# Optimization experiments

Measured on AMD Instinct MI355X. Metric: run time of the kernel, lower is better.

The kernel has to match this reference:

```python
import math
import jax, jax.numpy as jnp
import numpy as np

H, D, HID, BLOCK = 32, 64, 2048, 256   # heads, head_dim, hidden(=h*d), chunk size
N = 8192                                # prefill sequence length
NUM_LAYERS, LAYER_IDX = 80, 0
EPS = 1e-5


def _build_slopes(n):
    def p2(m):
        start = 2 ** (-2 ** (-(math.log2(m) - 3)))
        return [start * start ** i for i in range(m)]
    if math.log2(n).is_integer():
        s = p2(n)
    else:
        cp = 2 ** math.floor(math.log2(n))
        s = p2(cp) + _build_slopes(2 * cp).tolist()[0::2][: n - cp]
    return np.array(s, dtype=np.float32)

SLOPE = jnp.asarray(_build_slopes(H) * (1.0 - LAYER_IDX / (NUM_LAYERS - 1) + 1e-5))  # [H]


def setup_inputs() -> dict:
    key = jax.random.key(0)
    ks = jax.random.split(key, 5)
    return {
        "hidden_states": jax.random.normal(ks[0], (N, HID), jnp.float32),
        "kv_cache": jnp.zeros((H, D, D), jnp.float32),
        "W_qkv": jax.random.normal(ks[1], (3 * HID, HID), jnp.float32) * 0.02,
        "W_gate": jax.random.normal(ks[2], (HID, HID), jnp.float32) * 0.02,
        "W_out": jax.random.normal(ks[3], (HID, HID), jnp.float32) * 0.02,
        "norm_weight": jnp.ones((HID,), jnp.float32),
    }


def lightning_attention(q, k, v, slope, kv0):
    # q,k,v: [h,n,d]; kv0: [h,d,d]; chunked linear attention with per-head decay
    h, n, d = q.shape
    nb = n // BLOCK
    arr = jnp.arange(BLOCK, dtype=jnp.float32) + 1.0          # 1..BLOCK
    s = slope[:, None, None]                                   # [h,1,1]
    q_decay = jnp.exp(-s * arr[None, :, None])                 # [h,B,1]
    k_decay = jnp.exp(-s * (BLOCK - arr)[None, :, None])       # [h,B,1]
    idx = arr[:, None] - arr[None, :]                          # [B,B]
    diag_decay = jnp.where(idx[None] >= 0, jnp.exp(-s * idx[None]), 0.0)  # [h,B,B]
    block_decay = jnp.exp(-slope * BLOCK)[:, None, None]       # [h,1,1]

    def to_blocks(x):
        return x.reshape(h, nb, BLOCK, d).transpose(1, 0, 2, 3)  # [nb,h,B,d]

    qb, kb, vb = to_blocks(q), to_blocks(k), to_blocks(v)

    def step(kv, blk):
        qi, ki, vi = blk                                        # [h,B,d]
        inter = jnp.einsum('hmd,hde->hme', qi * q_decay, kv)    # carry-state term
        qk = jnp.einsum('hmd,hnd->hmn', qi, ki) * diag_decay    # intra-block causal decayed scores
        intra = jnp.einsum('hmn,hne->hme', qk, vi)
        kv_new = block_decay * kv + jnp.einsum('hmd,hme->hde', ki * k_decay, vi)
        return kv_new, inter + intra

    kv_final, out = jax.lax.scan(step, kv0, (qb, kb, vb))
    out = out.transpose(1, 0, 2, 3).reshape(h, n, d)
    return out, kv_final


def reference(hidden_states, kv_cache, W_qkv, W_gate, W_out, norm_weight):
    # qkv projection + SiLU in fp32 (as in vLLM MiniMaxText01)
    qkv = jax.nn.silu((hidden_states @ W_qkv.T).astype(jnp.float32))  # [n, 3*HID]
    qkv = qkv.reshape(N, H, 3 * D)
    q, k, v = jnp.split(qkv, 3, axis=-1)                              # each [n,h,d]
    q, k, v = (t.transpose(1, 0, 2) for t in (q, k, v))               # [h,n,d]
    attn, _kv = lightning_attention(q, k, v, SLOPE, kv_cache)
    hidden = attn.transpose(1, 0, 2).reshape(N, H * D)                # 'h n d -> n (h d)'
    # RMSNorm (tp_world=1)
    var = jnp.mean(hidden * hidden, axis=-1, keepdims=True)
    hidden = hidden * jax.lax.rsqrt(var + EPS) * norm_weight
    gate = jax.nn.sigmoid(hidden_states @ W_gate.T)
    return (gate * hidden) @ W_out.T
```

## Files before the change

### kernel.cpp

```cpp
#include <hip/hip_runtime.h>

#define NTOK   8192
#define HIDDEN 2048
#define NHEAD  32
#define HDIM   64
#define BLK    256
#define NBLK   32
#define QKVW   6144

typedef unsigned short ushort_t;
typedef __attribute__((ext_vector_type(8))) short bf16x8;
typedef __attribute__((ext_vector_type(4))) float floatx4;
typedef __attribute__((ext_vector_type(4))) unsigned short ushortx4;

#define MFMA16(a, b, c) __builtin_amdgcn_mfma_f32_16x16x32_bf16(a, b, c, 0, 0, 0)

__device__ __forceinline__ float head_slope(int h) {
    return exp2f(-0.25f * (float)(h + 1)) * 1.00001f;
}

__device__ __forceinline__ ushort_t f2bf(float x) {
    unsigned int u = __float_as_uint(x);
    unsigned int r = (u + 0x7FFFu + ((u >> 16) & 1u)) >> 16;
    return (ushort_t)r;
}
__device__ __forceinline__ float bf2f(ushort_t x) {
    return __uint_as_float(((unsigned int)x) << 16);
}
__device__ __forceinline__ void store1(float* p, float v) { *p = v; }
__device__ __forceinline__ void store1(ushort_t* p, float v) { *p = f2bf(v); }

#define GLOAD_LDS16(g, l)                                              \
    __builtin_amdgcn_global_load_lds(                                  \
        (const __attribute__((address_space(1))) void*)(g),            \
        (__attribute__((address_space(3))) void*)(l), 16, 0, 0)

__global__ __launch_bounds__(256) void cvt_bf16(
    const float* __restrict__ in, ushort_t* __restrict__ out, int n8) {
    int i = blockIdx.x * 256 + threadIdx.x;
    if (i >= n8) return;
    long base = (long)i * 8;
    float4 a = *(const float4*)(in + base);
    float4 b = *(const float4*)(in + base + 4);
    ushort4 u0 = {f2bf(a.x), f2bf(a.y), f2bf(a.z), f2bf(a.w)};
    ushort4 u1 = {f2bf(b.x), f2bf(b.y), f2bf(b.z), f2bf(b.w)};
    *(ushort4*)(out + base) = u0;
    *(ushort4*)(out + base + 4) = u1;
}

template <int EPI, typename OutT>
__global__ __launch_bounds__(512, 2) void gemm256_bt(
    const ushort_t* __restrict__ A, const ushort_t* __restrict__ B,
    OutT* __restrict__ C, const float* __restrict__ Mul,
    int M, int Ncol, int K) {
    __shared__ __align__(128) ushort_t As[3][256 * 32];
    __shared__ __align__(128) ushort_t Bs[3][256 * 32];

    const int t = threadIdx.x;
    const int wave = t >> 6, lane = t & 63;
    const int wm = wave >> 2, wn = wave & 3;
    const int fm = lane & 15, quad = lane >> 4;
    const int pcol = (quad ^ ((fm >> 1) & 3)) << 3;

    const int nbn = Ncol >> 8;
    const int flat = blockIdx.y * gridDim.x + blockIdx.x;
    const int nwg = gridDim.x * gridDim.y;
    const int nid = (flat & 7) * (nwg >> 3) + (flat >> 3);
    const int bm = nid / nbn, bn = nid % nbn;

    const int sr = t >> 2;
    const int sc = (((t & 3) ^ ((t >> 3) & 3))) << 3;
    const ushort_t* Ag0 = A + (long)(bm * 256 + sr) * K + sc;
    const ushort_t* Ag1 = Ag0 + (long)128 * K;
    const ushort_t* Bg0 = B + (long)(bn * 256 + sr) * K + sc;
    const ushort_t* Bg1 = Bg0 + (long)128 * K;
    const int ldst = wave * 512;

#define STAGE256(kt_, buf_)                                            \
    do {                                                               \
        const long ko_ = (long)(kt_) * 32;                             \
        GLOAD_LDS16(Ag0 + ko_, &As[buf_][ldst]);                       \
        GLOAD_LDS16(Ag1 + ko_, &As[buf_][4096 + ldst]);                \
        GLOAD_LDS16(Bg0 + ko_, &Bs[buf_][ldst]);                       \
        GLOAD_LDS16(Bg1 + ko_, &Bs[buf_][4096 + ldst]);                \
    } while (0)

    floatx4 acc[8][4];
#pragma unroll
    for (int i = 0; i < 8; i++)
#pragma unroll
        for (int j = 0; j < 4; j++) acc[i][j] = (floatx4){0.f, 0.f, 0.f, 0.f};

    const int NKT = K >> 5;
    STAGE256(0, 0);
    STAGE256(1, 1);
    asm volatile("s_waitcnt vmcnt(4)" ::: "memory");
    __builtin_amdgcn_s_barrier();

    int cur = 0;
    for (int kt = 0; kt < NKT; ++kt) {
        const ushort_t* Ab = As[cur];
        const ushort_t* Bb = Bs[cur];
        int sb = cur + 2; if (sb >= 3) sb -= 3;
        const bool do_stage = (kt + 2 < NKT);

        bf16x8 af[4], bfr[4];
#pragma unroll
        for (int mt = 0; mt < 4; ++mt)
            af[mt] = *(const bf16x8*)&Ab[(wm * 128 + mt * 16 + fm) * 32 + pcol];
#pragma unroll
        for (int nt = 0; nt < 4; ++nt)
            bfr[nt] = *(const bf16x8*)&Bb[(wn * 64 + nt * 16 + fm) * 32 + pcol];
        if (do_stage) {
            const long ko = (long)(kt + 2) * 32;
            GLOAD_LDS16(Ag0 + ko, &As[sb][ldst]);
            GLOAD_LDS16(Ag1 + ko, &As[sb][4096 + ldst]);
        }
        asm volatile("s_waitcnt lgkmcnt(0)" ::: "memory");
        __builtin_amdgcn_sched_barrier(0);
        __builtin_amdgcn_s_setprio(1);
#pragma unroll
        for (int mt = 0; mt < 4; ++mt)
#pragma unroll
            for (int nt = 0; nt < 4; ++nt)
                acc[mt][nt] = MFMA16(af[mt], bfr[nt], acc[mt][nt]);
        __builtin_amdgcn_s_setprio(0);
        __builtin_amdgcn_s_barrier();

#pragma unroll
        for (int mt = 0; mt < 4; ++mt)
            af[mt] = *(const bf16x8*)&Ab[(wm * 128 + 64 + mt * 16 + fm) * 32 + pcol];
        if (do_stage) {
            const long ko = (long)(kt + 2) * 32;
            GLOAD_LDS16(Bg0 + ko, &Bs[sb][ldst]);
            GLOAD_LDS16(Bg1 + ko, &Bs[sb][4096 + ldst]);
        }
        asm volatile("s_waitcnt lgkmcnt(0)" ::: "memory");
        __builtin_amdgcn_sched_barrier(0);
        __builtin_amdgcn_s_setprio(1);
#pragma unroll
        for (int mt = 0; mt < 4; ++mt)
#pragma unroll
            for (int nt = 0; nt < 4; ++nt)
                acc[4 + mt][nt] = MFMA16(af[mt], bfr[nt], acc[4 + mt][nt]);
        __builtin_amdgcn_s_setprio(0);

        if (kt + 2 < NKT) {
            asm volatile("s_waitcnt vmcnt(4)" ::: "memory");
            __builtin_amdgcn_s_barrier();
        } else if (kt + 1 < NKT) {
            asm volatile("s_waitcnt vmcnt(0)" ::: "memory");
            __builtin_amdgcn_s_barrier();
        }
        cur = sb - 1; if (cur < 0) cur = 2;
    }
#undef STAGE256

#pragma unroll
    for (int mh = 0; mh < 2; ++mh)
#pragma unroll
        for (int mt = 0; mt < 4; ++mt)
#pragma unroll
            for (int nt = 0; nt < 4; ++nt) {
                long col = (long)bn * 256 + wn * 64 + nt * 16 + fm;
#pragma unroll
                for (int r = 0; r < 4; ++r) {
                    long row = (long)bm * 256 + wm * 128 + mh * 64 + mt * 16 +
                               quad * 4 + r;
                    long idx = row * Ncol + col;
                    float x = acc[mh * 4 + mt][nt][r];
                    float o;
                    if (EPI == 0)      o = x / (1.f + expf(-x));
                    else if (EPI == 1) o = x;
                    else               o = Mul[idx] / (1.f + expf(-x));
                    store1(C + idx, o);
                }
            }
}

__global__ __launch_bounds__(256) void attn_contrib_mfma(
    const ushort_t* __restrict__ qkv, float* __restrict__ contrib) {
    const int b = blockIdx.x, h = blockIdx.y;
    const float s = head_slope(h);
    __shared__ ushort_t kdT[64][72];
    __shared__ ushort_t vT[64][72];
    const int t = threadIdx.x, wave = t >> 6, lane = t & 63;
    const int fm = lane & 15, quad = lane >> 4;
    const ushort_t* base = qkv + (long)(b * BLK) * QKVW + h * (3 * HDIM);

    floatx4 acc[4];
#pragma unroll
    for (int e = 0; e < 4; e++) acc[e] = (floatx4){0.f, 0.f, 0.f, 0.f};

    const int sn = t & 63;
    const int sc0 = t >> 6;

    for (int tt = 0; tt < 4; tt++) {
        __syncthreads();
        int tok = tt * 64 + sn;
        float kd = expf(-s * (float)(BLK - 1 - tok));
#pragma unroll
        for (int cc = 0; cc < 2; cc++) {
            int c = sc0 + cc * 4;
            bf16x8 k8 = *(const bf16x8*)(base + (long)tok * QKVW + HDIM + c * 8);
            bf16x8 v8 = *(const bf16x8*)(base + (long)tok * QKVW + 2 * HDIM + c * 8);
#pragma unroll
            for (int j = 0; j < 8; j++) {
                kdT[c * 8 + j][sn] = f2bf(bf2f((ushort_t)k8[j]) * kd);
                vT[c * 8 + j][sn]  = (ushort_t)v8[j];
            }
        }
        __syncthreads();
#pragma unroll
        for (int kh = 0; kh < 2; kh++) {
            bf16x8 a = *(const bf16x8*)&kdT[wave * 16 + fm][kh * 32 + quad * 8];
#pragma unroll
            for (int e = 0; e < 4; e++) {
                bf16x8 bb = *(const bf16x8*)&vT[e * 16 + fm][kh * 32 + quad * 8];
                acc[e] = MFMA16(a, bb, acc[e]);
            }
        }
    }
    float* outp = contrib + ((long)(h * NBLK + b)) * 4096;
#pragma unroll
    for (int e = 0; e < 4; e++)
#pragma unroll
        for (int r = 0; r < 4; r++) {
            int d = wave * 16 + quad * 4 + r;
            outp[d * 64 + e * 16 + fm] = acc[e][r];
        }
}

__global__ __launch_bounds__(256) void attn_scan(
    const float* __restrict__ kv0, const float* __restrict__ contrib,
    float* __restrict__ states) {
    const int h = blockIdx.x, t = threadIdx.x;
    const float s  = head_slope(h);
    const float bd = expf(-s * (float)BLK);
    float st[16], c[16];
    const float* kvp = kv0 + (long)h * 4096;
#pragma unroll
    for (int i = 0; i < 16; i++) st[i] = kvp[t + 256 * i];
    for (int b = 0; b < NBLK; b++) {
        const float* cp = contrib + ((long)(h * NBLK + b)) * 4096;
        float* sp = states + ((long)(h * NBLK + b)) * 4096;
#pragma unroll
        for (int i = 0; i < 16; i++) c[i] = cp[t + 256 * i];
#pragma unroll
        for (int i = 0; i < 16; i++) sp[t + 256 * i] = st[i];
#pragma unroll
        for (int i = 0; i < 16; i++) st[i] = bd * st[i] + c[i];
    }
}

__global__ __launch_bounds__(256) void attn_core_mfma(
    const ushort_t* __restrict__ qkv, const float* __restrict__ states,
    float* __restrict__ hidden) {
    const int b = blockIdx.x, h = blockIdx.y;
    const float s = head_slope(h);
    __shared__ ushort_t Sw[4][64][72];
    __shared__ ushort_t kS[64 * 64];
    __shared__ ushort_t vT[64][72];
    __shared__ float dtab[257];
    __shared__ float etab[64];
    const int t = threadIdx.x, wave = t >> 6, lane = t & 63;
    const int fm = lane & 15, quad = lane >> 4;
    const ushort_t* base = qkv + (long)(b * BLK) * QKVW + h * (3 * HDIM);

    dtab[t] = expf(-s * (float)t);
    if (t == 0) dtab[256] = expf(-s * 256.f);
    if (t < 64) etab[t] = expf(s * (float)t);

    {
        const float* sp = states + ((long)(h * NBLK + b)) * 4096;
#pragma unroll
        for (int i = 0; i < 4; i++) {
            int idx = t + 256 * i;
            int d = idx >> 4, e4 = (idx & 15) * 4;
            float4 st4 = *(const float4*)(sp + d * 64 + e4);
            Sw[0][e4 + 0][d] = f2bf(st4.x);
            Sw[0][e4 + 1][d] = f2bf(st4.y);
            Sw[0][e4 + 2][d] = f2bf(st4.z);
            Sw[0][e4 + 3][d] = f2bf(st4.w);
        }
    }

    bf16x8 aq[4][2];
#pragma unroll
    for (int mt = 0; mt < 4; mt++)
#pragma unroll
        for (int kh = 0; kh < 2; kh++)
            aq[mt][kh] = *(const bf16x8*)(base +
                (long)(wave * 64 + mt * 16 + fm) * QKVW + kh * 32 + quad * 8);

    __syncthreads();

    floatx4 acc[4][4];
#pragma unroll
    for (int i = 0; i < 4; i++)
#pragma unroll
        for (int j = 0; j < 4; j++) acc[i][j] = (floatx4){0.f, 0.f, 0.f, 0.f};
#pragma unroll
    for (int kh = 0; kh < 2; kh++)
#pragma unroll
        for (int et = 0; et < 4; et++) {
            bf16x8 bst = *(const bf16x8*)&Sw[0][et * 16 + fm][kh * 32 + quad * 8];
#pragma unroll
            for (int mt = 0; mt < 4; mt++)
                acc[mt][et] = MFMA16(aq[mt][kh], bst, acc[mt][et]);
        }
#pragma unroll
    for (int mt = 0; mt < 4; mt++)
#pragma unroll
        for (int r = 0; r < 4; r++) {
            float qd = dtab[wave * 64 + mt * 16 + quad * 4 + r + 1];
#pragma unroll
            for (int et = 0; et < 4; et++) acc[mt][et][r] *= qd;
        }

    const int sn = t & 63, sc0 = t >> 6;
    for (int nt = 0; nt < 4; nt++) {
        __syncthreads();
#pragma unroll
        for (int i = 0; i < 2; i++) {
            int row = i * 32 + wave * 8 + (lane >> 3);
            const ushort_t* g = base + (long)(nt * 64 + row) * QKVW + HDIM +
                                (((lane & 7) ^ (lane >> 3)) * 8);
            GLOAD_LDS16(g, &kS[(i * 32 + wave * 8) * 64]);
        }
#pragma unroll
        for (int cc = 0; cc < 2; cc++) {
            int c = sc0 + cc * 4;
            bf16x8 v8 = *(const bf16x8*)(base + (long)(nt * 64 + sn) * QKVW +
                                         2 * HDIM + c * 8);
#pragma unroll
            for (int j = 0; j < 8; j++) vT[c * 8 + j][sn] = (ushort_t)v8[j];
        }
        __syncthreads();

        if (nt <= wave) {
            floatx4 sacc[4][4];
#pragma unroll
            for (int i = 0; i < 4; i++)
#pragma unroll
                for (int j = 0; j < 4; j++) sacc[i][j] = (floatx4){0.f, 0.f, 0.f, 0.f};
#pragma unroll
            for (int kh = 0; kh < 2; kh++) {
                bf16x8 ak[4];
#pragma unroll
                for (int snt = 0; snt < 4; snt++) {
                    int n = snt * 16 + fm;
                    int pos = (kh * 4 + quad) ^ (n & 7);
                    ak[snt] = *(const bf16x8*)&kS[n * 64 + pos * 8];
                }
#pragma unroll
                for (int snt = 0; snt < 4; snt++)
#pragma unroll
                    for (int smt = 0; smt < 4; smt++)
                        sacc[snt][smt] = MFMA16(ak[snt], aq[smt][kh], sacc[snt][smt]);
            }
#pragma unroll
            for (int snt = 0; snt < 4; snt++)
#pragma unroll
                for (int smt = 0; smt < 4; smt++) {
                    int mloc = smt * 16 + fm;
                    float rf = dtab[wave * 64 + mloc - nt * 64];
                    ushortx4 o;
#pragma unroll
                    for (int r = 0; r < 4; r++) {
                        int nloc = snt * 16 + quad * 4 + r;
                        float v = sacc[snt][smt][r] * rf * etab[nloc];
                        if (nt == wave && mloc < nloc) v = 0.f;
                        o[r] = f2bf(v);
                    }
                    *(ushortx4*)&Sw[wave][mloc][snt * 16 + quad * 4] = o;
                }
#pragma unroll
            for (int kh = 0; kh < 2; kh++) {
                bf16x8 as[4];
#pragma unroll
                for (int mt = 0; mt < 4; mt++)
                    as[mt] = *(const bf16x8*)&Sw[wave][mt * 16 + fm][kh * 32 + quad * 8];
#pragma unroll
                for (int et = 0; et < 4; et++) {
                    bf16x8 bv = *(const bf16x8*)&vT[et * 16 + fm][kh * 32 + quad * 8];
#pragma unroll
                    for (int mt = 0; mt < 4; mt++)
                        acc[mt][et] = MFMA16(as[mt], bv, acc[mt][et]);
                }
            }
        }
    }

#pragma unroll
    for (int mt = 0; mt < 4; mt++)
#pragma unroll
        for (int r = 0; r < 4; r++) {
            long tok = (long)b * BLK + wave * 64 + mt * 16 + quad * 4 + r;
            float* hp = hidden + tok * HIDDEN + h * HDIM;
#pragma unroll
            for (int et = 0; et < 4; et++)
                hp[et * 16 + fm] = acc[mt][et][r];
        }
}

__global__ __launch_bounds__(256) void rmsnorm_rows(
    float* __restrict__ hidden, const float* __restrict__ w) {
    const int row = blockIdx.x, t = threadIdx.x;
    float* hp = hidden + (long)row * HIDDEN;
    float4 a = *(const float4*)(hp + (t << 2));
    float4 b = *(const float4*)(hp + 1024 + (t << 2));
    float ss = a.x * a.x + a.y * a.y + a.z * a.z + a.w * a.w +
               b.x * b.x + b.y * b.y + b.z * b.z + b.w * b.w;
#pragma unroll
    for (int off = 32; off > 0; off >>= 1) ss += __shfl_down(ss, off);
    __shared__ float red[4];
    if ((t & 63) == 0) red[t >> 6] = ss;
    __syncthreads();
    float tot = red[0] + red[1] + red[2] + red[3];
    float scale = rsqrtf(tot * (1.f / HIDDEN) + 1e-5f);
    float4 wa = *(const float4*)(w + (t << 2));
    float4 wb = *(const float4*)(w + 1024 + (t << 2));
    a.x *= scale * wa.x; a.y *= scale * wa.y; a.z *= scale * wa.z; a.w *= scale * wa.w;
    b.x *= scale * wb.x; b.y *= scale * wb.y; b.z *= scale * wb.z; b.w *= scale * wb.w;
    *(float4*)(hp + (t << 2)) = a;
    *(float4*)(hp + 1024 + (t << 2)) = b;
}

extern "C" void kernel_launch(void* const* d_in, const int* in_sizes, int n_in,
                              void* d_out, int out_size, void* d_ws, size_t ws_size,
                              hipStream_t stream) {
    (void)in_sizes; (void)n_in; (void)out_size; (void)ws_size;
    const float* hs   = (const float*)d_in[0];
    const float* kv0  = (const float*)d_in[1];
    const float* Wqkv = (const float*)d_in[2];
    const float* Wg   = (const float*)d_in[3];
    const float* Wo   = (const float*)d_in[4];
    const float* nw   = (const float*)d_in[5];
    float* out = (float*)d_out;

    ushort_t* hs_h   = (ushort_t*)d_ws;
    ushort_t* wqkv_h = hs_h + (size_t)NTOK * HIDDEN;
    ushort_t* wg_h   = wqkv_h + (size_t)QKVW * HIDDEN;
    ushort_t* wo_h   = wg_h + (size_t)HIDDEN * HIDDEN;
    ushort_t* qkv_h  = wo_h + (size_t)HIDDEN * HIDDEN;
    float*    cs     = (float*)(qkv_h + (size_t)NTOK * QKVW);
    ushort_t* gated  = qkv_h;

    cvt_bf16<<<(NTOK * HIDDEN / 8 + 255) / 256, 256, 0, stream>>>(
        hs, hs_h, NTOK * HIDDEN / 8);
    cvt_bf16<<<(QKVW * HIDDEN / 8 + 255) / 256, 256, 0, stream>>>(
        Wqkv, wqkv_h, QKVW * HIDDEN / 8);
    cvt_bf16<<<(HIDDEN * HIDDEN / 8 + 255) / 256, 256, 0, stream>>>(
        Wg, wg_h, HIDDEN * HIDDEN / 8);
    cvt_bf16<<<(HIDDEN * HIDDEN / 8 + 255) / 256, 256, 0, stream>>>(
        Wo, wo_h, HIDDEN * HIDDEN / 8);

    gemm256_bt<0, ushort_t><<<dim3(QKVW / 256, NTOK / 256), 512, 0, stream>>>(
        hs_h, wqkv_h, qkv_h, nullptr, NTOK, QKVW, HIDDEN);
    attn_contrib_mfma<<<dim3(NBLK, NHEAD), 256, 0, stream>>>(qkv_h, cs);
    attn_scan<<<NHEAD, 256, 0, stream>>>(kv0, cs, cs);
    attn_core_mfma<<<dim3(NBLK, NHEAD), 256, 0, stream>>>(qkv_h, cs, out);
    rmsnorm_rows<<<NTOK, 256, 0, stream>>>(out, nw);
    gemm256_bt<2, ushort_t><<<dim3(HIDDEN / 256, NTOK / 256), 512, 0, stream>>>(
        hs_h, wg_h, gated, out, NTOK, HIDDEN, HIDDEN);
    gemm256_bt<1, float><<<dim3(HIDDEN / 256, NTOK / 256), 512, 0, stream>>>(
        gated, wo_h, out, nullptr, NTOK, HIDDEN, HIDDEN);
}
```

Before: 694.7 us.

## Deepen GEMM LDS pipeline to four stages and reorder tile rasterization

Moves the bf16 GEMM from a 3-buffer to a 4-buffer LDS ring, prefetching three k-tiles ahead with matching vmcnt waits and extra barriers, so global-load latency has more time to hide. It also changes the workgroup-to-tile mapping to walk M first within each column of B tiles, and fixes the LDS swizzle to use the row index. LDS use grows to 128KB per workgroup, which may fall short of the two workgroups per CU that the launch bounds ask for, and the added barriers cost extra synchronization per k-step.

```diff
diff --git a/kernel.cpp b/kernel.cpp
--- a/kernel.cpp
+++ b/kernel.cpp
@@ -53,8 +53,8 @@
     const ushort_t* __restrict__ A, const ushort_t* __restrict__ B,
     OutT* __restrict__ C, const float* __restrict__ Mul,
     int M, int Ncol, int K) {
-    __shared__ __align__(128) ushort_t As[3][256 * 32];
-    __shared__ __align__(128) ushort_t Bs[3][256 * 32];
+    __shared__ __align__(128) ushort_t As[4][256 * 32];
+    __shared__ __align__(128) ushort_t Bs[4][256 * 32];
 
     const int t = threadIdx.x;
     const int wave = t >> 6, lane = t & 63;
@@ -62,25 +62,30 @@
     const int fm = lane & 15, quad = lane >> 4;
     const int pcol = (quad ^ ((fm >> 1) & 3)) << 3;
 
-    const int nbn = Ncol >> 8;
     const int flat = blockIdx.y * gridDim.x + blockIdx.x;
     const int nwg = gridDim.x * gridDim.y;
     const int nid = (flat & 7) * (nwg >> 3) + (flat >> 3);
-    const int bm = nid / nbn, bn = nid % nbn;
+    const int nbm = M >> 8;
+    const int bn = nid / nbm;
+    const int bm = nid - bn * nbm;
 
     const int sr = t >> 2;
-    const int sc = (((t & 3) ^ ((t >> 3) & 3))) << 3;
+    const int sc = ((t & 3) ^ ((sr >> 1) & 3)) << 3;
     const ushort_t* Ag0 = A + (long)(bm * 256 + sr) * K + sc;
     const ushort_t* Ag1 = Ag0 + (long)128 * K;
     const ushort_t* Bg0 = B + (long)(bn * 256 + sr) * K + sc;
     const ushort_t* Bg1 = Bg0 + (long)128 * K;
     const int ldst = wave * 512;
 
-#define STAGE256(kt_, buf_)                                            \
+#define STAGE_A(kt_, buf_)                                             \
     do {                                                               \
         const long ko_ = (long)(kt_) * 32;                             \
         GLOAD_LDS16(Ag0 + ko_, &As[buf_][ldst]);                       \
         GLOAD_LDS16(Ag1 + ko_, &As[buf_][4096 + ldst]);                \
+    } while (0)
+#define STAGE_B(kt_, buf_)                                             \
+    do {                                                               \
+        const long ko_ = (long)(kt_) * 32;                             \
         GLOAD_LDS16(Bg0 + ko_, &Bs[buf_][ldst]);                       \
         GLOAD_LDS16(Bg1 + ko_, &Bs[buf_][4096 + ldst]);                \
     } while (0)
@@ -92,17 +97,17 @@
         for (int j = 0; j < 4; j++) acc[i][j] = (floatx4){0.f, 0.f, 0.f, 0.f};
 
     const int NKT = K >> 5;
-    STAGE256(0, 0);
-    STAGE256(1, 1);
-    asm volatile("s_waitcnt vmcnt(4)" ::: "memory");
+    STAGE_A(0, 0); STAGE_B(0, 0);
+    STAGE_A(1, 1); STAGE_B(1, 1);
+    STAGE_A(2, 2); STAGE_B(2, 2);
+    asm volatile("s_waitcnt vmcnt(8)" ::: "memory");
     __builtin_amdgcn_s_barrier();
 
-    int cur = 0;
     for (int kt = 0; kt < NKT; ++kt) {
-        const ushort_t* Ab = As[cur];
-        const ushort_t* Bb = Bs[cur];
-        int sb = cur + 2; if (sb >= 3) sb -= 3;
-        const bool do_stage = (kt + 2 < NKT);
+        const ushort_t* Ab = As[kt & 3];
+        const ushort_t* Bb = Bs[kt & 3];
+        const int sb = (kt + 3) & 3;
+        const bool do_stage = (kt + 3 < NKT);
 
         bf16x8 af[4], bfr[4];
 #pragma unroll
@@ -111,11 +116,8 @@
 #pragma unroll
         for (int nt = 0; nt < 4; ++nt)
             bfr[nt] = *(const bf16x8*)&Bb[(wn * 64 + nt * 16 + fm) * 32 + pcol];
-        if (do_stage) {
-            const long ko = (long)(kt + 2) * 32;
-            GLOAD_LDS16(Ag0 + ko, &As[sb][ldst]);
-            GLOAD_LDS16(Ag1 + ko, &As[sb][4096 + ldst]);
-        }
+        if (do_stage) STAGE_A(kt + 3, sb);
+        __builtin_amdgcn_s_barrier();
         asm volatile("s_waitcnt lgkmcnt(0)" ::: "memory");
         __builtin_amdgcn_sched_barrier(0);
         __builtin_amdgcn_s_setprio(1);
@@ -130,11 +132,8 @@
 #pragma unroll
         for (int mt = 0; mt < 4; ++mt)
             af[mt] = *(const bf16x8*)&Ab[(wm * 128 + 64 + mt * 16 + fm) * 32 + pcol];
-        if (do_stage) {
-            const long ko = (long)(kt + 2) * 32;
-            GLOAD_LDS16(Bg0 + ko, &Bs[sb][ldst]);
-            GLOAD_LDS16(Bg1 + ko, &Bs[sb][4096 + ldst]);
-        }
+        if (do_stage) STAGE_B(kt + 3, sb);
+        __builtin_amdgcn_s_barrier();
         asm volatile("s_waitcnt lgkmcnt(0)" ::: "memory");
         __builtin_amdgcn_sched_barrier(0);
         __builtin_amdgcn_s_setprio(1);
@@ -145,16 +144,17 @@
                 acc[4 + mt][nt] = MFMA16(af[mt], bfr[nt], acc[4 + mt][nt]);
         __builtin_amdgcn_s_setprio(0);
 
-        if (kt + 2 < NKT) {
+        if (kt + 3 < NKT) {
+            asm volatile("s_waitcnt vmcnt(8)" ::: "memory");
+        } else if (kt + 2 < NKT) {
             asm volatile("s_waitcnt vmcnt(4)" ::: "memory");
-            __builtin_amdgcn_s_barrier();
         } else if (kt + 1 < NKT) {
             asm volatile("s_waitcnt vmcnt(0)" ::: "memory");
-            __builtin_amdgcn_s_barrier();
-        }
-        cur = sb - 1; if (cur < 0) cur = 2;
+        }
+        __builtin_amdgcn_s_barrier();
     }
-#undef STAGE256
+#undef STAGE_A
+#undef STAGE_B
 
 #pragma unroll
     for (int mh = 0; mh < 2; ++mh)
```

Result: slower. 720.0 us (+3.6%).

## Restructure bf16 GEMM to K=64 tiles, double buffering and four-phase MFMA schedule

Applied to the files above, without the earlier changes.

The 256x256 bf16 GEMM mainloop now uses K-tiles of 64 instead of 32, with two LDS buffers instead of three and an XOR swizzle over 8 chunks. Each iteration is split into four MFMA quadrants, and the global-to-LDS loads for tile kt+2 are interleaved between quadrants so memory traffic overlaps compute and there are fewer loop iterations and barriers per K. The LDS footprint stays at 128KB. The cost is more barriers inside each iteration and a more fragile schedule, since the buffer being read is partly refilled while other quadrants still use it.

```diff
diff --git a/kernel.cpp b/kernel.cpp
--- a/kernel.cpp
+++ b/kernel.cpp
@@ -53,37 +53,38 @@
     const ushort_t* __restrict__ A, const ushort_t* __restrict__ B,
     OutT* __restrict__ C, const float* __restrict__ Mul,
     int M, int Ncol, int K) {
-    __shared__ __align__(128) ushort_t As[3][256 * 32];
-    __shared__ __align__(128) ushort_t Bs[3][256 * 32];
+    __shared__ __align__(128) ushort_t As[2][256 * 64];
+    __shared__ __align__(128) ushort_t Bs[2][256 * 64];
 
     const int t = threadIdx.x;
     const int wave = t >> 6, lane = t & 63;
     const int wm = wave >> 2, wn = wave & 3;
     const int fm = lane & 15, quad = lane >> 4;
-    const int pcol = (quad ^ ((fm >> 1) & 3)) << 3;
 
     const int nbn = Ncol >> 8;
     const int flat = blockIdx.y * gridDim.x + blockIdx.x;
     const int nwg = gridDim.x * gridDim.y;
     const int nid = (flat & 7) * (nwg >> 3) + (flat >> 3);
-    const int bm = nid / nbn, bn = nid % nbn;
-
-    const int sr = t >> 2;
-    const int sc = (((t & 3) ^ ((t >> 3) & 3))) << 3;
-    const ushort_t* Ag0 = A + (long)(bm * 256 + sr) * K + sc;
-    const ushort_t* Ag1 = Ag0 + (long)128 * K;
-    const ushort_t* Bg0 = B + (long)(bn * 256 + sr) * K + sc;
-    const ushort_t* Bg1 = Bg0 + (long)128 * K;
-    const int ldst = wave * 512;
-
-#define STAGE256(kt_, buf_)                                            \
-    do {                                                               \
-        const long ko_ = (long)(kt_) * 32;                             \
-        GLOAD_LDS16(Ag0 + ko_, &As[buf_][ldst]);                       \
-        GLOAD_LDS16(Ag1 + ko_, &As[buf_][4096 + ldst]);                \
-        GLOAD_LDS16(Bg0 + ko_, &Bs[buf_][ldst]);                       \
-        GLOAD_LDS16(Bg1 + ko_, &Bs[buf_][4096 + ldst]);                \
-    } while (0)
+    const int bm = nid / nbn;
+    const int bn = nid - bm * nbn;
+
+    const int srow = t >> 3;
+    const int schunk = ((t & 7) ^ (srow & 7)) << 3;
+    const ushort_t* Ags = A + ((long)bm * 256 + srow) * K + schunk;
+    const ushort_t* Bgs = B + ((long)bn * 256 + srow) * K + schunk;
+    const int sdst = wave * 512;
+
+#define STAGE_AQ(kt_, buf_, q_)                                          \
+    GLOAD_LDS16(Ags + (long)(q_) * 64 * K + (long)(kt_) * 64,            \
+                &As[buf_][(q_) * 4096 + sdst])
+#define STAGE_BQ(kt_, buf_, q_)                                          \
+    GLOAD_LDS16(Bgs + (long)(q_) * 64 * K + (long)(kt_) * 64,            \
+                &Bs[buf_][(q_) * 4096 + sdst])
+
+    const int aoff = (wm * 128 + fm) * 64;
+    const int boff = (wn * 64 + fm) * 64;
+    const int cx0 = ((quad ^ (fm & 7)) << 3);
+    const int cx1 = (((4 + quad) ^ (fm & 7)) << 3);
 
     floatx4 acc[8][4];
 #pragma unroll
@@ -91,91 +92,133 @@
 #pragma unroll
         for (int j = 0; j < 4; j++) acc[i][j] = (floatx4){0.f, 0.f, 0.f, 0.f};
 
-    const int NKT = K >> 5;
-    STAGE256(0, 0);
-    STAGE256(1, 1);
-    asm volatile("s_waitcnt vmcnt(4)" ::: "memory");
+    const int NKT = K >> 6;
+#pragma unroll
+    for (int q = 0; q < 4; q++) STAGE_AQ(0, 0, q);
+#pragma unroll
+    for (int q = 0; q < 4; q++) STAGE_BQ(0, 0, q);
+#pragma unroll
+    for (int q = 0; q < 4; q++) STAGE_AQ(1, 1, q);
+#pragma unroll
+    for (int q = 0; q < 4; q++) STAGE_BQ(1, 1, q);
+    asm volatile("s_waitcnt vmcnt(8)" ::: "memory");
     __builtin_amdgcn_s_barrier();
 
-    int cur = 0;
     for (int kt = 0; kt < NKT; ++kt) {
-        const ushort_t* Ab = As[cur];
-        const ushort_t* Bb = Bs[cur];
-        int sb = cur + 2; if (sb >= 3) sb -= 3;
-        const bool do_stage = (kt + 2 < NKT);
-
-        bf16x8 af[4], bfr[4];
-#pragma unroll
-        for (int mt = 0; mt < 4; ++mt)
-            af[mt] = *(const bf16x8*)&Ab[(wm * 128 + mt * 16 + fm) * 32 + pcol];
-#pragma unroll
-        for (int nt = 0; nt < 4; ++nt)
-            bfr[nt] = *(const bf16x8*)&Bb[(wn * 64 + nt * 16 + fm) * 32 + pcol];
-        if (do_stage) {
-            const long ko = (long)(kt + 2) * 32;
-            GLOAD_LDS16(Ag0 + ko, &As[sb][ldst]);
-            GLOAD_LDS16(Ag1 + ko, &As[sb][4096 + ldst]);
-        }
+        const int cur = kt & 1;
+        const ushort_t* Ab = &As[cur][0];
+        const ushort_t* Bb = &Bs[cur][0];
+        const bool st = (kt + 2 < NKT);
+
+        bf16x8 a0[4][2], a1[4][2], bl[2][2], bh[2][2];
+
+#pragma unroll
+        for (int mt = 0; mt < 4; ++mt) {
+            a0[mt][0] = *(const bf16x8*)&Ab[aoff + mt * 1024 + cx0];
+            a0[mt][1] = *(const bf16x8*)&Ab[aoff + mt * 1024 + cx1];
+        }
+#pragma unroll
+        for (int nt = 0; nt < 2; ++nt) {
+            bl[nt][0] = *(const bf16x8*)&Bb[boff + nt * 1024 + cx0];
+            bl[nt][1] = *(const bf16x8*)&Bb[boff + nt * 1024 + cx1];
+        }
+        __builtin_amdgcn_s_barrier();
         asm volatile("s_waitcnt lgkmcnt(0)" ::: "memory");
         __builtin_amdgcn_sched_barrier(0);
         __builtin_amdgcn_s_setprio(1);
 #pragma unroll
         for (int mt = 0; mt < 4; ++mt)
 #pragma unroll
-            for (int nt = 0; nt < 4; ++nt)
-                acc[mt][nt] = MFMA16(af[mt], bfr[nt], acc[mt][nt]);
+            for (int nt = 0; nt < 2; ++nt) {
+                acc[mt][nt] = MFMA16(a0[mt][0], bl[nt][0], acc[mt][nt]);
+                acc[mt][nt] = MFMA16(a0[mt][1], bl[nt][1], acc[mt][nt]);
+            }
         __builtin_amdgcn_s_setprio(0);
         __builtin_amdgcn_s_barrier();
 
 #pragma unroll
-        for (int mt = 0; mt < 4; ++mt)
-            af[mt] = *(const bf16x8*)&Ab[(wm * 128 + 64 + mt * 16 + fm) * 32 + pcol];
-        if (do_stage) {
-            const long ko = (long)(kt + 2) * 32;
-            GLOAD_LDS16(Bg0 + ko, &Bs[sb][ldst]);
-            GLOAD_LDS16(Bg1 + ko, &Bs[sb][4096 + ldst]);
-        }
+        for (int nt = 0; nt < 2; ++nt) {
+            bh[nt][0] = *(const bf16x8*)&Bb[boff + 2048 + nt * 1024 + cx0];
+            bh[nt][1] = *(const bf16x8*)&Bb[boff + 2048 + nt * 1024 + cx1];
+        }
+        if (st) { STAGE_AQ(kt + 2, cur, 0); STAGE_AQ(kt + 2, cur, 2); }
+        __builtin_amdgcn_s_barrier();
         asm volatile("s_waitcnt lgkmcnt(0)" ::: "memory");
         __builtin_amdgcn_sched_barrier(0);
         __builtin_amdgcn_s_setprio(1);
 #pragma unroll
         for (int mt = 0; mt < 4; ++mt)
 #pragma unroll
-            for (int nt = 0; nt < 4; ++nt)
-                acc[4 + mt][nt] = MFMA16(af[mt], bfr[nt], acc[4 + mt][nt]);
+            for (int nt = 0; nt < 2; ++nt) {
+                acc[mt][2 + nt] = MFMA16(a0[mt][0], bh[nt][0], acc[mt][2 + nt]);
+                acc[mt][2 + nt] = MFMA16(a0[mt][1], bh[nt][1], acc[mt][2 + nt]);
+            }
         __builtin_amdgcn_s_setprio(0);
+        __builtin_amdgcn_s_barrier();
+
+#pragma unroll
+        for (int mt = 0; mt < 4; ++mt) {
+            a1[mt][0] = *(const bf16x8*)&Ab[aoff + 4096 + mt * 1024 + cx0];
+            a1[mt][1] = *(const bf16x8*)&Ab[aoff + 4096 + mt * 1024 + cx1];
+        }
+        if (st) {
+            STAGE_BQ(kt + 2, cur, 0); STAGE_BQ(kt + 2, cur, 1);
+            STAGE_BQ(kt + 2, cur, 2); STAGE_BQ(kt + 2, cur, 3);
+        }
+        __builtin_amdgcn_s_barrier();
+        asm volatile("s_waitcnt lgkmcnt(0)" ::: "memory");
+        __builtin_amdgcn_sched_barrier(0);
+        __builtin_amdgcn_s_setprio(1);
+#pragma unroll
+        for (int mt = 0; mt < 4; ++mt)
+#pragma unroll
+            for (int nt = 0; nt < 2; ++nt) {
+                acc[4 + mt][2 + nt] = MFMA16(a1[mt][0], bh[nt][0], acc[4 + mt][2 + nt]);
+                acc[4 + mt][2 + nt] = MFMA16(a1[mt][1], bh[nt][1], acc[4 + mt][2 + nt]);
+            }
+        __builtin_amdgcn_s_setprio(0);
+        __builtin_amdgcn_s_barrier();
+
+        if (st) { STAGE_AQ(kt + 2, cur, 1); STAGE_AQ(kt + 2, cur, 3); }
+        __builtin_amdgcn_s_barrier();
+        __builtin_amdgcn_sched_barrier(0);
+        __builtin_amdgcn_s_setprio(1);
+#pragma unroll
+        for (int mt = 0; mt < 4; ++mt)
+#pragma unroll
+            for (int nt = 0; nt < 2; ++nt) {
+                acc[4 + mt][nt] = MFMA16(a1[mt][0], bl[nt][0], acc[4 + mt][nt]);
+                acc[4 + mt][nt] = MFMA16(a1[mt][1], bl[nt][1], acc[4 + mt][nt]);
+            }
+        __builtin_amdgcn_s_setprio(0);
 
         if (kt + 2 < NKT) {
-            asm volatile("s_waitcnt vmcnt(4)" ::: "memory");
-            __builtin_amdgcn_s_barrier();
+            asm volatile("s_waitcnt vmcnt(8)" ::: "memory");
         } else if (kt + 1 < NKT) {
             asm volatile("s_waitcnt vmcnt(0)" ::: "memory");
-            __builtin_amdgcn_s_barrier();
-        }
-        cur = sb - 1; if (cur < 0) cur = 2;
+        }
+        __builtin_amdgcn_s_barrier();
     }
-#undef STAGE256
-
-#pragma unroll
-    for (int mh = 0; mh < 2; ++mh)
-#pragma unroll
-        for (int mt = 0; mt < 4; ++mt)
-#pragma unroll
-            for (int nt = 0; nt < 4; ++nt) {
-                long col = (long)bn * 256 + wn * 64 + nt * 16 + fm;
-#pragma unroll
-                for (int r = 0; r < 4; ++r) {
-                    long row = (long)bm * 256 + wm * 128 + mh * 64 + mt * 16 +
-                               quad * 4 + r;
-                    long idx = row * Ncol + col;
-                    float x = acc[mh * 4 + mt][nt][r];
-                    float o;
-                    if (EPI == 0)      o = x / (1.f + expf(-x));
-                    else if (EPI == 1) o = x;
-                    else               o = Mul[idx] / (1.f + expf(-x));
-                    store1(C + idx, o);
-                }
-            }
+#undef STAGE_AQ
+#undef STAGE_BQ
+
+#pragma unroll
+    for (int mt = 0; mt < 8; ++mt)
+#pragma unroll
+        for (int nt = 0; nt < 4; ++nt) {
+            long col = (long)bn * 256 + wn * 64 + nt * 16 + fm;
+#pragma unroll
+            for (int r = 0; r < 4; ++r) {
+                long row = (long)bm * 256 + wm * 128 + mt * 16 + quad * 4 + r;
+                long idx = row * Ncol + col;
+                float x = acc[mt][nt][r];
+                float o;
+                if (EPI == 0)      o = x / (1.f + expf(-x));
+                else if (EPI == 1) o = x;
+                else               o = Mul[idx] / (1.f + expf(-x));
+                store1(C + idx, o);
+            }
+        }
 }
 
 __global__ __launch_bounds__(256) void attn_contrib_mfma(
```

After: 676.1 us. 1.03x faster.
